# Performance work log

Measured on AMD Instinct MI355X. Metric: run time of the kernel, lower is better.

Reference implementation:

```python
import jax, jax.numpy as jnp
import numpy as np

BN_EPS = 1e-5


def _batchnorm(x, gamma, beta):
    # training-mode BatchNorm2d: biased batch stats over (N, H, W)
    mean = jnp.mean(x, axis=(0, 2, 3), keepdims=True)
    var = jnp.var(x, axis=(0, 2, 3), keepdims=True)
    xn = (x - mean) * jax.lax.rsqrt(var + BN_EPS)
    return xn * gamma[None, :, None, None] + beta[None, :, None, None]


def _bin_weight(w):
    # BitConv2d_Robust: w_bin = sign(w) * mean(|w|) per output channel (STE in fwd is just the value)
    alpha = jnp.mean(jnp.abs(w), axis=(1, 2, 3), keepdims=True)
    return jax.lax.stop_gradient(jnp.sign(w) * alpha - w) + w


def _conv(x, w, b, pad):
    y = jax.lax.conv_general_dilated(
        x, w, window_strides=(1, 1), padding=[(pad, pad), (pad, pad)],
        dimension_numbers=('NCHW', 'OIHW', 'NCHW'))
    return y + b[None, :, None, None]


def setup_inputs() -> dict:
    key = jax.random.key(0)
    ks = jax.random.split(key, 14)
    B, Cin, Cout, T, H, W = 16, 128, 256, 512, 64, 64
    fan1 = Cin * 9
    fan2 = Cout * 9
    return {
        'x': jax.random.normal(ks[0], (B, Cin, H, W), jnp.float32),
        't': jax.random.normal(ks[1], (B, T), jnp.float32),
        'bn1_g': jnp.ones((Cin,), jnp.float32),
        'bn1_b': jnp.zeros((Cin,), jnp.float32),
        'w1': jax.random.normal(ks[2], (Cout, Cin, 3, 3), jnp.float32) / np.sqrt(fan1),
        'b1': jax.random.normal(ks[3], (Cout,), jnp.float32) * 0.01,
        'tW': jax.random.normal(ks[4], (Cout, T), jnp.float32) / np.sqrt(T),
        'tb': jax.random.normal(ks[5], (Cout,), jnp.float32) * 0.01,
        'bn2_g': jnp.ones((Cout,), jnp.float32),
        'bn2_b': jnp.zeros((Cout,), jnp.float32),
        'w2': jax.random.normal(ks[6], (Cout, Cout, 3, 3), jnp.float32) / np.sqrt(fan2),
        'b2': jax.random.normal(ks[7], (Cout,), jnp.float32) * 0.01,
        'ws': jax.random.normal(ks[8], (Cout, Cin, 1, 1), jnp.float32) / np.sqrt(Cin),
        'bs': jax.random.normal(ks[9], (Cout,), jnp.float32) * 0.01,
    }


def reference(x, t, bn1_g, bn1_b, w1, b1, tW, tb, bn2_g, bn2_b, w2, b2, ws, bs):
    h = jnp.sign(_batchnorm(x, bn1_g, bn1_b))                # BN + sign binarize
    h = _conv(h, _bin_weight(w1), b1, pad=1)                  # binarized 3x3 conv
    temb = t @ tW.T + tb                                      # time MLP -> [B, Cout]
    h = h + temb[:, :, None, None]
    h = jnp.sign(_batchnorm(h, bn2_g, bn2_b))
    h = _conv(h, _bin_weight(w2), b2, pad=1)
    skip = _conv(x, _bin_weight(ws), bs, pad=0)               # 1x1 binarized skip (in_ch != out_ch)
    return h + skip
```

## Files before the change

### kernel.cpp

```cpp
#include <hip/hip_runtime.h>
#include <stdint.h>

typedef unsigned int uint;

#define EPS 1e-5f


__global__ __launch_bounds__(256) void k_bn1_part(const float* __restrict__ x, float* __restrict__ part) {
  int c = blockIdx.x, chunk = blockIdx.y;
  float s = 0.f, s2 = 0.f;
  #pragma unroll
  for (int jb = 0; jb < 2; ++jb) {
    int b = chunk * 2 + jb;
    const float4* xb = (const float4*)(x + (((size_t)((b << 7) | c)) << 12));
    #pragma unroll
    for (int k = 0; k < 4; ++k) {
      float4 q = xb[k * 256 + threadIdx.x];
      s += (q.x + q.y) + (q.z + q.w);
      s2 += q.x * q.x + q.y * q.y + q.z * q.z + q.w * q.w;
    }
  }
  #pragma unroll
  for (int off = 32; off > 0; off >>= 1) { s += __shfl_down(s, off); s2 += __shfl_down(s2, off); }
  __shared__ float ls[4], ls2[4];
  int wid = threadIdx.x >> 6, lane = threadIdx.x & 63;
  if (lane == 0) { ls[wid] = s; ls2[wid] = s2; }
  __syncthreads();
  if (threadIdx.x == 0) {
    part[(c * 8 + chunk) * 2 + 0] = ls[0] + ls[1] + ls[2] + ls[3];
    part[(c * 8 + chunk) * 2 + 1] = ls2[0] + ls2[1] + ls2[2] + ls2[3];
  }
}

__global__ void k_bn1_fin(const float* __restrict__ part, const float* __restrict__ g,
                          const float* __restrict__ be, float* __restrict__ sc, float* __restrict__ sh) {
  int c = threadIdx.x;
  float s = 0.f, s2 = 0.f;
  for (int k = 0; k < 8; ++k) { s += part[(c * 8 + k) * 2]; s2 += part[(c * 8 + k) * 2 + 1]; }
  const float inv = 1.f / 65536.f;
  float m = s * inv, var = s2 * inv - m * m;
  float rs = rsqrtf(var + EPS);
  float scale = rs * g[c];
  sc[c] = scale;
  sh[c] = be[c] - m * scale;
}

__global__ __launch_bounds__(128) void k_packw1(const float* __restrict__ w1, uint* __restrict__ wb,
                                                float* __restrict__ alpha) {
  int co = blockIdx.x, wid = threadIdx.x >> 6, lane = threadIdx.x & 63;
  const float* wp = w1 + (co * 128 + threadIdx.x) * 9;
  float wv[9]; float s = 0.f;
  #pragma unroll
  for (int tp = 0; tp < 9; ++tp) { wv[tp] = wp[tp]; s += fabsf(wv[tp]); }
  #pragma unroll
  for (int tp = 0; tp < 9; ++tp) {
    unsigned long long m = __ballot(wv[tp] > 0.f);
    if (lane == 0) {
      wb[(co * 9 + tp) * 4 + wid * 2 + 0] = (uint)m;
      wb[(co * 9 + tp) * 4 + wid * 2 + 1] = (uint)(m >> 32);
    }
  }
  #pragma unroll
  for (int off = 32; off > 0; off >>= 1) s += __shfl_down(s, off);
  __shared__ float l2[2];
  if (lane == 0) l2[wid] = s;
  __syncthreads();
  if (threadIdx.x == 0) alpha[co] = (l2[0] + l2[1]) * (1.f / 1152.f);
}

__global__ __launch_bounds__(256) void k_packw2(const float* __restrict__ w2, uint* __restrict__ wb,
                                                float* __restrict__ alpha) {
  int co = blockIdx.x, wid = threadIdx.x >> 6, lane = threadIdx.x & 63;
  const float* wp = w2 + (co * 256 + threadIdx.x) * 9;
  float wv[9]; float s = 0.f;
  #pragma unroll
  for (int tp = 0; tp < 9; ++tp) { wv[tp] = wp[tp]; s += fabsf(wv[tp]); }
  #pragma unroll
  for (int tp = 0; tp < 9; ++tp) {
    unsigned long long m = __ballot(wv[tp] > 0.f);
    if (lane == 0) {
      wb[(co * 9 + tp) * 8 + wid * 2 + 0] = (uint)m;
      wb[(co * 9 + tp) * 8 + wid * 2 + 1] = (uint)(m >> 32);
    }
  }
  #pragma unroll
  for (int off = 32; off > 0; off >>= 1) s += __shfl_down(s, off);
  __shared__ float l4[4];
  if (lane == 0) l4[wid] = s;
  __syncthreads();
  if (threadIdx.x == 0) alpha[co] = (l4[0] + l4[1] + l4[2] + l4[3]) * (1.f / 2304.f);
}

__global__ __launch_bounds__(256) void k_base(const uint* __restrict__ wb1, const uint* __restrict__ wb2,
                                              int* __restrict__ base1, int* __restrict__ base2) {
  int co = threadIdx.x;
  int pc1[9], pc2[9];
  #pragma unroll
  for (int tp = 0; tp < 9; ++tp) {
    uint a = 0;
    #pragma unroll
    for (int k = 0; k < 4; ++k) a += __popc(wb1[co * 36 + tp * 4 + k]);
    pc1[tp] = (int)a;
    uint b = 0;
    #pragma unroll
    for (int k = 0; k < 8; ++k) b += __popc(wb2[co * 72 + tp * 8 + k]);
    pc2[tp] = (int)b;
  }
  #pragma unroll
  for (int pat = 0; pat < 9; ++pat) {
    int yt = pat / 3, xt = pat % 3;
    int b1v = 1152, b2v = 2304;
    #pragma unroll
    for (int tp = 0; tp < 9; ++tp) {
      int dy = tp / 3 - 1, dx = tp % 3 - 1;
      bool inv = (dy < 0 && yt == 0) || (dy > 0 && yt == 2) || (dx < 0 && xt == 0) || (dx > 0 && xt == 2);
      if (inv) { b1v -= 128 - 2 * pc1[tp]; b2v -= 256 - 2 * pc2[tp]; }
    }
    base1[pat * 256 + co] = b1v;
    base2[pat * 256 + co] = b2v;
  }
}

__global__ __launch_bounds__(128) void k_packws(const float* __restrict__ wsk, float* __restrict__ swT) {
  int co = blockIdx.x, ci = threadIdx.x;
  float v = wsk[co * 128 + ci];
  float s = fabsf(v);
  #pragma unroll
  for (int off = 32; off > 0; off >>= 1) s += __shfl_down(s, off);
  __shared__ float l2[2]; __shared__ float tot;
  int wid = threadIdx.x >> 6, lane = threadIdx.x & 63;
  if (lane == 0) l2[wid] = s;
  __syncthreads();
  if (threadIdx.x == 0) tot = (l2[0] + l2[1]) * (1.f / 128.f);
  __syncthreads();
  float a = tot;
  swT[ci * 256 + co] = (v > 0.f) ? a : -a;
}

__global__ __launch_bounds__(256) void k_temb(const float* __restrict__ t, const float* __restrict__ tW,
                                              const float* __restrict__ tbias, float* __restrict__ temb) {
  int b = blockIdx.x, co = threadIdx.x;
  const float* tr = t + b * 512;
  const float* wr = tW + co * 512;
  float a0 = 0, a1 = 0, a2 = 0, a3 = 0;
  #pragma unroll 8
  for (int k = 0; k < 512; k += 4) {
    a0 = fmaf(tr[k + 0], wr[k + 0], a0);
    a1 = fmaf(tr[k + 1], wr[k + 1], a1);
    a2 = fmaf(tr[k + 2], wr[k + 2], a2);
    a3 = fmaf(tr[k + 3], wr[k + 3], a3);
  }
  temb[b * 256 + co] = (a0 + a1) + (a2 + a3) + tbias[co];
}

__global__ __launch_bounds__(256, 2) void k_skip(const float* __restrict__ x, const float* __restrict__ swT,
                                                 const float* __restrict__ bsk, const float* __restrict__ b2,
                                                 const float* __restrict__ sc1, const float* __restrict__ sh1,
                                                 uint* __restrict__ sbinw, float* __restrict__ out) {
  __shared__ float xs[128 * 64];
  __shared__ float wsl[128 * 64];
  int g = blockIdx.x;
  int b = g >> 6;
  int px0 = (g & 63) << 6;
  int co0 = blockIdx.y << 6;
  int t = threadIdx.x;

  {
    const float* xb = x + ((size_t)(b << 7) << 12) + px0;
    float4* xs4 = (float4*)xs;
    #pragma unroll
    for (int k = 0; k < 8; ++k) {
      int idx = k * 256 + t;
      int ci = idx >> 4, f4 = idx & 15;
      xs4[idx] = *(const float4*)(xb + ((size_t)ci << 12) + (f4 << 2));
    }
  }
  {
    float4* ws4 = (float4*)wsl;
    #pragma unroll
    for (int k = 0; k < 8; ++k) {
      int idx = k * 256 + t;
      int ci = idx >> 4, f4 = idx & 15;
      ws4[idx] = *(const float4*)(swT + ci * 256 + co0 + (f4 << 2));
    }
  }
  __syncthreads();

  if (blockIdx.y == 0) {
    int px = t & 63, wd = t >> 6;
    int ci0 = wd << 5;
    uint acc = 0;
    #pragma unroll
    for (int i = 0; i < 32; ++i) {
      int ci = ci0 + i;
      float v = xs[ci * 64 + px];
      acc |= ((v * sc1[ci] + sh1[ci]) > 0.f ? 1u : 0u) << i;
    }
    sbinw[(((size_t)b << 12) | (px0 + px)) * 4 + wd] = acc;
  }

  int tx = t & 15, ty = t >> 4;
  const float4* xs4 = (const float4*)xs;
  const float4* ws4 = (const float4*)wsl;
  float4 acc0 = make_float4(0, 0, 0, 0), acc1 = acc0, acc2 = acc0, acc3 = acc0;
  #pragma unroll 4
  for (int ci = 0; ci < 128; ++ci) {
    float4 xv = xs4[ci * 16 + tx];
    float4 wv = ws4[ci * 16 + ty];
    acc0.x = fmaf(wv.x, xv.x, acc0.x); acc0.y = fmaf(wv.x, xv.y, acc0.y);
    acc0.z = fmaf(wv.x, xv.z, acc0.z); acc0.w = fmaf(wv.x, xv.w, acc0.w);
    acc1.x = fmaf(wv.y, xv.x, acc1.x); acc1.y = fmaf(wv.y, xv.y, acc1.y);
    acc1.z = fmaf(wv.y, xv.z, acc1.z); acc1.w = fmaf(wv.y, xv.w, acc1.w);
    acc2.x = fmaf(wv.z, xv.x, acc2.x); acc2.y = fmaf(wv.z, xv.y, acc2.y);
    acc2.z = fmaf(wv.z, xv.z, acc2.z); acc2.w = fmaf(wv.z, xv.w, acc2.w);
    acc3.x = fmaf(wv.w, xv.x, acc3.x); acc3.y = fmaf(wv.w, xv.y, acc3.y);
    acc3.z = fmaf(wv.w, xv.z, acc3.z); acc3.w = fmaf(wv.w, xv.w, acc3.w);
  }

  float* op = out + ((size_t)b << 20) + px0 + (tx << 2);
  int cob = co0 + (ty << 2);
  float4 r;
  r = acc0; { float bb = bsk[cob + 0] + b2[cob + 0]; r.x += bb; r.y += bb; r.z += bb; r.w += bb; }
  *(float4*)(op + (size_t)(cob + 0) * 4096) = r;
  r = acc1; { float bb = bsk[cob + 1] + b2[cob + 1]; r.x += bb; r.y += bb; r.z += bb; r.w += bb; }
  *(float4*)(op + (size_t)(cob + 1) * 4096) = r;
  r = acc2; { float bb = bsk[cob + 2] + b2[cob + 2]; r.x += bb; r.y += bb; r.z += bb; r.w += bb; }
  *(float4*)(op + (size_t)(cob + 2) * 4096) = r;
  r = acc3; { float bb = bsk[cob + 3] + b2[cob + 3]; r.x += bb; r.y += bb; r.z += bb; r.w += bb; }
  *(float4*)(op + (size_t)(cob + 3) * 4096) = r;
}

__global__ __launch_bounds__(256, 1) void k_conv1(const uint4* __restrict__ sbin, const uint* __restrict__ wb1,
                                                  const int* __restrict__ base1, short* __restrict__ S1) {
  __shared__ uint wlds[32 * 36];
  __shared__ int blds[9 * 32];
  int co0 = blockIdx.y << 5;
  #pragma unroll
  for (int k = 0; k < 4; ++k) wlds[k * 256 + threadIdx.x] = wb1[co0 * 36 + k * 256 + threadIdx.x];
  if (threadIdx.x < 128) wlds[1024 + threadIdx.x] = wb1[co0 * 36 + 1024 + threadIdx.x];
  #pragma unroll
  for (int k = 0; k < 2; ++k) {
    int idx = k * 256 + threadIdx.x;
    if (idx < 288) blds[idx] = base1[(idx >> 5) * 256 + co0 + (idx & 31)];
  }

  int bt = blockIdx.x;
  int b = bt >> 4;
  int y = ((bt & 15) << 2) | (threadIdx.x >> 6);
  int cx = threadIdx.x & 63;
  uint nb[9][4];
  #pragma unroll
  for (int dy = -1; dy <= 1; ++dy)
    #pragma unroll
    for (int dx = -1; dx <= 1; ++dx) {
      int tp = (dy + 1) * 3 + (dx + 1);
      int yy = y + dy, xx = cx + dx;
      bool v = ((unsigned)yy < 64u) && ((unsigned)xx < 64u);
      uint4 q = make_uint4(0, 0, 0, 0);
      if (v) q = sbin[(b << 12) | (yy << 6) | xx];
      nb[tp][0] = q.x; nb[tp][1] = q.y; nb[tp][2] = q.z; nb[tp][3] = q.w;
    }
  int pat = ((y == 0) ? 0 : ((y == 63) ? 6 : 3)) + ((cx == 0) ? 0 : ((cx == 63) ? 2 : 1));
  __syncthreads();

  int p = (y << 6) | cx;
  short* op = S1 + ((size_t)b << 20) + ((size_t)co0 << 12) + p;
  #pragma unroll 1
  for (int cc = 0; cc < 4; ++cc) {
    short accv[8];
    #pragma unroll
    for (int j = 0; j < 8; ++j) {
      int co_l = cc * 8 + j;
      const uint4* wp4 = (const uint4*)(wlds + co_l * 36);
      uint m0 = 0, m1 = 0, m2 = 0, m3 = 0;
      #pragma unroll
      for (int tp = 0; tp < 9; ++tp) {
        uint4 w4 = wp4[tp];
        m0 += __popc(nb[tp][0] ^ w4.x);
        m1 += __popc(nb[tp][1] ^ w4.y);
        m2 += __popc(nb[tp][2] ^ w4.z);
        m3 += __popc(nb[tp][3] ^ w4.w);
      }
      accv[j] = (short)(blds[pat * 32 + co_l] - 2 * (int)((m0 + m1) + (m2 + m3)));
    }
    #pragma unroll
    for (int j = 0; j < 8; ++j) op[(size_t)(cc * 8 + j) << 12] = accv[j];
  }
}

__global__ __launch_bounds__(256) void k_bn2_part(const short* __restrict__ S1, const float* __restrict__ al1,
                                                  const float* __restrict__ b1, const float* __restrict__ temb,
                                                  float* __restrict__ part) {
  int co = blockIdx.x, chunk = blockIdx.y;
  float a = al1[co], bb = b1[co];
  float s = 0.f, s2 = 0.f;
  #pragma unroll
  for (int jb = 0; jb < 2; ++jb) {
    int b = chunk * 2 + jb;
    float tb_ = bb + temb[(b << 8) | co];
    const uint4* sp = (const uint4*)(S1 + ((size_t)b << 20) + ((size_t)co << 12));
    #pragma unroll
    for (int k = 0; k < 2; ++k) {
      uint4 q = sp[k * 256 + threadIdx.x];
      uint ws[4] = {q.x, q.y, q.z, q.w};
      #pragma unroll
      for (int w = 0; w < 4; ++w) {
        float f0 = fmaf(a, (float)((short)(ws[w] & 0xffffu)), tb_);
        float f1 = fmaf(a, (float)((short)(ws[w] >> 16)), tb_);
        s += f0 + f1;
        s2 += f0 * f0 + f1 * f1;
      }
    }
  }
  #pragma unroll
  for (int off = 32; off > 0; off >>= 1) { s += __shfl_down(s, off); s2 += __shfl_down(s2, off); }
  __shared__ float ls[4], ls2[4];
  int wid = threadIdx.x >> 6, lane = threadIdx.x & 63;
  if (lane == 0) { ls[wid] = s; ls2[wid] = s2; }
  __syncthreads();
  if (threadIdx.x == 0) {
    part[(co * 8 + chunk) * 2 + 0] = ls[0] + ls[1] + ls[2] + ls[3];
    part[(co * 8 + chunk) * 2 + 1] = ls2[0] + ls2[1] + ls2[2] + ls2[3];
  }
}

__global__ void k_bn2_fin(const float* __restrict__ part, const float* __restrict__ al1,
                          const float* __restrict__ b1, const float* __restrict__ g2,
                          const float* __restrict__ be2, float* __restrict__ A,
                          float* __restrict__ Bc, float* __restrict__ Cc) {
  int co = threadIdx.x;
  float s = 0.f, s2 = 0.f;
  for (int k = 0; k < 8; ++k) { s += part[(co * 8 + k) * 2]; s2 += part[(co * 8 + k) * 2 + 1]; }
  const float inv = 1.f / 65536.f;
  float m = s * inv, var = s2 * inv - m * m;
  float rs = rsqrtf(var + EPS);
  float gg = rs * g2[co];
  A[co] = al1[co] * gg;
  Bc[co] = (b1[co] - m) * gg + be2[co];
  Cc[co] = gg;
}

__global__ __launch_bounds__(256) void k_bin2(const short* __restrict__ S1, const float* __restrict__ A,
                                              const float* __restrict__ Bc, const float* __restrict__ Cc,
                                              const float* __restrict__ temb, uint4* __restrict__ hbin) {
  int pg = blockIdx.x * 256 + threadIdx.x;
  int b = pg >> 12, p = pg & 4095;
  int c0 = blockIdx.y << 7;
  const short* sp = S1 + ((size_t)b << 20) + p;
  const float* tp = temb + (b << 8);
  uint w[4];
  #pragma unroll
  for (int wd = 0; wd < 4; ++wd) {
    uint acc = 0;
    #pragma unroll
    for (int i = 0; i < 32; ++i) {
      int co = c0 + wd * 32 + i;
      float v = A[co] * (float)sp[(size_t)co << 12] + Bc[co] + Cc[co] * tp[co];
      acc |= (v > 0.f ? 1u : 0u) << i;
    }
    w[wd] = acc;
  }
  hbin[pg * 2 + blockIdx.y] = make_uint4(w[0], w[1], w[2], w[3]);
}

__global__ __launch_bounds__(256, 1) void k_conv2(const uint4* __restrict__ hbin, const uint* __restrict__ wb2,
                                                  const int* __restrict__ base2, const float* __restrict__ al2,
                                                  float* __restrict__ out) {
  __shared__ uint wlds[32 * 72];
  __shared__ int blds[9 * 32];
  int co0 = blockIdx.y << 5;
  #pragma unroll
  for (int k = 0; k < 9; ++k) wlds[k * 256 + threadIdx.x] = wb2[co0 * 72 + k * 256 + threadIdx.x];
  #pragma unroll
  for (int k = 0; k < 2; ++k) {
    int idx = k * 256 + threadIdx.x;
    if (idx < 288) blds[idx] = base2[(idx >> 5) * 256 + co0 + (idx & 31)];
  }

  int bt = blockIdx.x;
  int b = bt >> 4;
  int y = ((bt & 15) << 2) | (threadIdx.x >> 6);
  int cx = threadIdx.x & 63;
  uint nb[9][8];
  #pragma unroll
  for (int dy = -1; dy <= 1; ++dy)
    #pragma unroll
    for (int dx = -1; dx <= 1; ++dx) {
      int tp = (dy + 1) * 3 + (dx + 1);
      int yy = y + dy, xx = cx + dx;
      bool v = ((unsigned)yy < 64u) && ((unsigned)xx < 64u);
      uint4 q0 = make_uint4(0, 0, 0, 0), q1 = make_uint4(0, 0, 0, 0);
      if (v) {
        int pix = (b << 12) | (yy << 6) | xx;
        q0 = hbin[pix * 2 + 0];
        q1 = hbin[pix * 2 + 1];
      }
      nb[tp][0] = q0.x; nb[tp][1] = q0.y; nb[tp][2] = q0.z; nb[tp][3] = q0.w;
      nb[tp][4] = q1.x; nb[tp][5] = q1.y; nb[tp][6] = q1.z; nb[tp][7] = q1.w;
    }
  int pat = ((y == 0) ? 0 : ((y == 63) ? 6 : 3)) + ((cx == 0) ? 0 : ((cx == 63) ? 2 : 1));
  __syncthreads();

  int p = (y << 6) | cx;
  float* op = out + ((size_t)b << 20) + ((size_t)co0 << 12) + p;
  #pragma unroll 1
  for (int cc = 0; cc < 4; ++cc) {
    float ov[8];
    #pragma unroll
    for (int j = 0; j < 8; ++j) ov[j] = op[(size_t)(cc * 8 + j) << 12];
    #pragma unroll
    for (int j = 0; j < 8; ++j) {
      int co_l = cc * 8 + j;
      const uint4* wp4 = (const uint4*)(wlds + co_l * 72);
      uint m0 = 0, m1 = 0, m2 = 0, m3 = 0;
      #pragma unroll
      for (int tp = 0; tp < 9; ++tp) {
        uint4 wa = wp4[tp * 2 + 0];
        uint4 wb_ = wp4[tp * 2 + 1];
        m0 += __popc(nb[tp][0] ^ wa.x);
        m1 += __popc(nb[tp][1] ^ wa.y);
        m2 += __popc(nb[tp][2] ^ wa.z);
        m3 += __popc(nb[tp][3] ^ wa.w);
        m0 += __popc(nb[tp][4] ^ wb_.x);
        m1 += __popc(nb[tp][5] ^ wb_.y);
        m2 += __popc(nb[tp][6] ^ wb_.z);
        m3 += __popc(nb[tp][7] ^ wb_.w);
      }
      int acc = blds[pat * 32 + co_l] - 2 * (int)((m0 + m1) + (m2 + m3));
      ov[j] = fmaf(al2[co0 + co_l], (float)acc, ov[j]);
    }
    #pragma unroll
    for (int j = 0; j < 8; ++j) op[(size_t)(cc * 8 + j) << 12] = ov[j];
  }
}

extern "C" void kernel_launch(void* const* d_in, const int* in_sizes, int n_in,
                              void* d_out, int out_size, void* d_ws, size_t ws_size,
                              hipStream_t stream) {
  const float* x    = (const float*)d_in[0];
  const float* t    = (const float*)d_in[1];
  const float* bn1g = (const float*)d_in[2];
  const float* bn1b = (const float*)d_in[3];
  const float* w1   = (const float*)d_in[4];
  const float* b1   = (const float*)d_in[5];
  const float* tW   = (const float*)d_in[6];
  const float* tb   = (const float*)d_in[7];
  const float* bn2g = (const float*)d_in[8];
  const float* bn2b = (const float*)d_in[9];
  const float* w2   = (const float*)d_in[10];
  const float* b2   = (const float*)d_in[11];
  const float* wsk  = (const float*)d_in[12];
  const float* bsk  = (const float*)d_in[13];
  float* out = (float*)d_out;
  char* ws = (char*)d_ws;

  float* bn1part = (float*)(ws + 0);
  float* sc1     = (float*)(ws + 8192);
  float* sh1     = (float*)(ws + 8704);
  uint4* sbin    = (uint4*)(ws + 9216);
  uint*  wb1     = (uint*) (ws + 1057792);
  float* al1     = (float*)(ws + 1094656);
  uint*  wb2     = (uint*) (ws + 1095680);
  float* al2     = (float*)(ws + 1169408);
  float* swkT    = (float*)(ws + 1170432);
  float* temb    = (float*)(ws + 1301504);
  float* bn2part = (float*)(ws + 1317888);
  float* A2      = (float*)(ws + 1334272);
  float* Bc2     = (float*)(ws + 1335296);
  float* Cc2     = (float*)(ws + 1336320);
  uint4* hbin    = (uint4*)(ws + 1337344);
  int*   base1g  = (int*)  (ws + 3434496);
  int*   base2g  = (int*)  (ws + 3443712);
  short* S1      = (short*)(ws + 3452928);

  k_bn1_part<<<dim3(128, 8), 256, 0, stream>>>(x, bn1part);
  k_bn1_fin<<<1, 128, 0, stream>>>(bn1part, bn1g, bn1b, sc1, sh1);
  k_packw1<<<256, 128, 0, stream>>>(w1, wb1, al1);
  k_packw2<<<256, 256, 0, stream>>>(w2, wb2, al2);
  k_base<<<1, 256, 0, stream>>>(wb1, wb2, base1g, base2g);
  k_packws<<<256, 128, 0, stream>>>(wsk, swkT);
  k_temb<<<16, 256, 0, stream>>>(t, tW, tb, temb);
  k_skip<<<dim3(1024, 4), 256, 0, stream>>>(x, swkT, bsk, b2, sc1, sh1, (uint*)sbin, out);
  k_conv1<<<dim3(256, 8), 256, 0, stream>>>(sbin, wb1, base1g, S1);
  k_bn2_part<<<dim3(256, 8), 256, 0, stream>>>(S1, al1, b1, temb, bn2part);
  k_bn2_fin<<<1, 256, 0, stream>>>(bn2part, al1, b1, bn2g, bn2b, A2, Bc2, Cc2);
  k_bin2<<<dim3(256, 2), 256, 0, stream>>>(S1, A2, Bc2, Cc2, temb, hbin);
  k_conv2<<<dim3(256, 8), 256, 0, stream>>>(hbin, wb2, base2g, al2, out);
}
```

Before: 259.7 us.

## Read binary conv weights via uniform global loads and raise occupancy in conv kernels

```diff
diff --git a/kernel.cpp b/kernel.cpp
--- a/kernel.cpp
+++ b/kernel.cpp
@@ -230,19 +230,12 @@
   *(float4*)(op + (size_t)(cob + 3) * 4096) = r;
 }
 
-__global__ __launch_bounds__(256, 1) void k_conv1(const uint4* __restrict__ sbin, const uint* __restrict__ wb1,
+__global__ __launch_bounds__(256, 4) void k_conv1(const uint4* __restrict__ sbin, const uint* __restrict__ wb1,
                                                   const int* __restrict__ base1, short* __restrict__ S1) {
-  __shared__ uint wlds[32 * 36];
   __shared__ int blds[9 * 32];
   int co0 = blockIdx.y << 5;
-  #pragma unroll
-  for (int k = 0; k < 4; ++k) wlds[k * 256 + threadIdx.x] = wb1[co0 * 36 + k * 256 + threadIdx.x];
-  if (threadIdx.x < 128) wlds[1024 + threadIdx.x] = wb1[co0 * 36 + 1024 + threadIdx.x];
-  #pragma unroll
-  for (int k = 0; k < 2; ++k) {
-    int idx = k * 256 + threadIdx.x;
-    if (idx < 288) blds[idx] = base1[(idx >> 5) * 256 + co0 + (idx & 31)];
-  }
+  if (threadIdx.x < 256) blds[threadIdx.x] = base1[(threadIdx.x >> 5) * 256 + co0 + (threadIdx.x & 31)];
+  if (threadIdx.x < 32) blds[256 + threadIdx.x] = base1[8 * 256 + co0 + threadIdx.x];
 
   int bt = blockIdx.x;
   int b = bt >> 4;
@@ -263,28 +256,31 @@
   int pat = ((y == 0) ? 0 : ((y == 63) ? 6 : 3)) + ((cx == 0) ? 0 : ((cx == 63) ? 2 : 1));
   __syncthreads();
 
+  int accv[32];
+  #pragma unroll
+  for (int co_l = 0; co_l < 32; ++co_l) {
+    const uint4* wp = (const uint4*)(wb1 + (size_t)(co0 + co_l) * 36);
+    uint m0 = 0, m1 = 0, m2 = 0, m3 = 0;
+    #pragma unroll
+    for (int tp = 0; tp < 9; ++tp) {
+      uint4 w4 = wp[tp];
+      m0 += __popc(nb[tp][0] ^ w4.x);
+      m1 += __popc(nb[tp][1] ^ w4.y);
+      m2 += __popc(nb[tp][2] ^ w4.z);
+      m3 += __popc(nb[tp][3] ^ w4.w);
+    }
+    accv[co_l] = (int)((m0 + m1) + (m2 + m3));
+  }
+
   int p = (y << 6) | cx;
   short* op = S1 + ((size_t)b << 20) + ((size_t)co0 << 12) + p;
   #pragma unroll 1
   for (int cc = 0; cc < 4; ++cc) {
-    short accv[8];
     #pragma unroll
     for (int j = 0; j < 8; ++j) {
       int co_l = cc * 8 + j;
-      const uint4* wp4 = (const uint4*)(wlds + co_l * 36);
-      uint m0 = 0, m1 = 0, m2 = 0, m3 = 0;
-      #pragma unroll
-      for (int tp = 0; tp < 9; ++tp) {
-        uint4 w4 = wp4[tp];
-        m0 += __popc(nb[tp][0] ^ w4.x);
-        m1 += __popc(nb[tp][1] ^ w4.y);
-        m2 += __popc(nb[tp][2] ^ w4.z);
-        m3 += __popc(nb[tp][3] ^ w4.w);
-      }
-      accv[j] = (short)(blds[pat * 32 + co_l] - 2 * (int)((m0 + m1) + (m2 + m3)));
-    }
-    #pragma unroll
-    for (int j = 0; j < 8; ++j) op[(size_t)(cc * 8 + j) << 12] = accv[j];
+      op[(size_t)co_l << 12] = (short)(blds[pat * 32 + co_l] - 2 * accv[co_l]);
+    }
   }
 }
 
@@ -363,43 +359,54 @@
   hbin[pg * 2 + blockIdx.y] = make_uint4(w[0], w[1], w[2], w[3]);
 }
 
-__global__ __launch_bounds__(256, 1) void k_conv2(const uint4* __restrict__ hbin, const uint* __restrict__ wb2,
+__global__ __launch_bounds__(256, 4) void k_conv2(const uint4* __restrict__ hbin, const uint* __restrict__ wb2,
                                                   const int* __restrict__ base2, const float* __restrict__ al2,
                                                   float* __restrict__ out) {
-  __shared__ uint wlds[32 * 72];
   __shared__ int blds[9 * 32];
+  __shared__ float alds[32];
   int co0 = blockIdx.y << 5;
-  #pragma unroll
-  for (int k = 0; k < 9; ++k) wlds[k * 256 + threadIdx.x] = wb2[co0 * 72 + k * 256 + threadIdx.x];
-  #pragma unroll
-  for (int k = 0; k < 2; ++k) {
-    int idx = k * 256 + threadIdx.x;
-    if (idx < 288) blds[idx] = base2[(idx >> 5) * 256 + co0 + (idx & 31)];
-  }
+  if (threadIdx.x < 256) blds[threadIdx.x] = base2[(threadIdx.x >> 5) * 256 + co0 + (threadIdx.x & 31)];
+  if (threadIdx.x < 32) blds[256 + threadIdx.x] = base2[8 * 256 + co0 + threadIdx.x];
+  if (threadIdx.x >= 32 && threadIdx.x < 64) alds[threadIdx.x - 32] = al2[co0 + threadIdx.x - 32];
 
   int bt = blockIdx.x;
   int b = bt >> 4;
   int y = ((bt & 15) << 2) | (threadIdx.x >> 6);
   int cx = threadIdx.x & 63;
-  uint nb[9][8];
-  #pragma unroll
-  for (int dy = -1; dy <= 1; ++dy)
-    #pragma unroll
-    for (int dx = -1; dx <= 1; ++dx) {
-      int tp = (dy + 1) * 3 + (dx + 1);
-      int yy = y + dy, xx = cx + dx;
-      bool v = ((unsigned)yy < 64u) && ((unsigned)xx < 64u);
-      uint4 q0 = make_uint4(0, 0, 0, 0), q1 = make_uint4(0, 0, 0, 0);
-      if (v) {
-        int pix = (b << 12) | (yy << 6) | xx;
-        q0 = hbin[pix * 2 + 0];
-        q1 = hbin[pix * 2 + 1];
+  int pat = ((y == 0) ? 0 : ((y == 63) ? 6 : 3)) + ((cx == 0) ? 0 : ((cx == 63) ? 2 : 1));
+  __syncthreads();
+
+  int accv[32];
+  #pragma unroll
+  for (int hc = 0; hc < 2; ++hc) {
+    uint nb[9][4];
+    #pragma unroll
+    for (int dy = -1; dy <= 1; ++dy)
+      #pragma unroll
+      for (int dx = -1; dx <= 1; ++dx) {
+        int tp = (dy + 1) * 3 + (dx + 1);
+        int yy = y + dy, xx = cx + dx;
+        bool v = ((unsigned)yy < 64u) && ((unsigned)xx < 64u);
+        uint4 q = make_uint4(0, 0, 0, 0);
+        if (v) q = hbin[(((b << 12) | (yy << 6) | xx) << 1) + hc];
+        nb[tp][0] = q.x; nb[tp][1] = q.y; nb[tp][2] = q.z; nb[tp][3] = q.w;
       }
-      nb[tp][0] = q0.x; nb[tp][1] = q0.y; nb[tp][2] = q0.z; nb[tp][3] = q0.w;
-      nb[tp][4] = q1.x; nb[tp][5] = q1.y; nb[tp][6] = q1.z; nb[tp][7] = q1.w;
-    }
-  int pat = ((y == 0) ? 0 : ((y == 63) ? 6 : 3)) + ((cx == 0) ? 0 : ((cx == 63) ? 2 : 1));
-  __syncthreads();
+    #pragma unroll
+    for (int co_l = 0; co_l < 32; ++co_l) {
+      const uint4* wp = (const uint4*)(wb2 + (size_t)(co0 + co_l) * 72) + hc;
+      uint m0 = 0, m1 = 0, m2 = 0, m3 = 0;
+      #pragma unroll
+      for (int tp = 0; tp < 9; ++tp) {
+        uint4 w4 = wp[tp * 2];
+        m0 += __popc(nb[tp][0] ^ w4.x);
+        m1 += __popc(nb[tp][1] ^ w4.y);
+        m2 += __popc(nb[tp][2] ^ w4.z);
+        m3 += __popc(nb[tp][3] ^ w4.w);
+      }
+      int mm = (int)((m0 + m1) + (m2 + m3));
+      if (hc == 0) accv[co_l] = mm; else accv[co_l] += mm;
+    }
+  }
 
   int p = (y << 6) | cx;
   float* op = out + ((size_t)b << 20) + ((size_t)co0 << 12) + p;
@@ -411,23 +418,8 @@
     #pragma unroll
     for (int j = 0; j < 8; ++j) {
       int co_l = cc * 8 + j;
-      const uint4* wp4 = (const uint4*)(wlds + co_l * 72);
-      uint m0 = 0, m1 = 0, m2 = 0, m3 = 0;
-      #pragma unroll
-      for (int tp = 0; tp < 9; ++tp) {
-        uint4 wa = wp4[tp * 2 + 0];
-        uint4 wb_ = wp4[tp * 2 + 1];
-        m0 += __popc(nb[tp][0] ^ wa.x);
-        m1 += __popc(nb[tp][1] ^ wa.y);
-        m2 += __popc(nb[tp][2] ^ wa.z);
-        m3 += __popc(nb[tp][3] ^ wa.w);
-        m0 += __popc(nb[tp][4] ^ wb_.x);
-        m1 += __popc(nb[tp][5] ^ wb_.y);
-        m2 += __popc(nb[tp][6] ^ wb_.z);
-        m3 += __popc(nb[tp][7] ^ wb_.w);
-      }
-      int acc = blds[pat * 32 + co_l] - 2 * (int)((m0 + m1) + (m2 + m3));
-      ov[j] = fmaf(al2[co0 + co_l], (float)acc, ov[j]);
+      int acc = blds[pat * 32 + co_l] - 2 * accv[co_l];
+      ov[j] = fmaf(alds[co_l], (float)acc, ov[j]);
     }
     #pragma unroll
     for (int j = 0; j < 8; ++j) op[(size_t)(cc * 8 + j) << 12] = ov[j];
```

Measured after the change: 518.2 us. +99.5%, slower.

## Replace popcount conv2 with bf16 MFMA conv on ±1 activations and weights

Applied to the files above, without the earlier changes.

```diff
diff --git a/kernel.cpp b/kernel.cpp
--- a/kernel.cpp
+++ b/kernel.cpp
@@ -2,6 +2,8 @@
 #include <stdint.h>
 
 typedef unsigned int uint;
+typedef short bf16x8 __attribute__((ext_vector_type(8)));
+typedef float f32x4 __attribute__((ext_vector_type(4)));
 
 #define EPS 1e-5f
 
@@ -69,7 +71,7 @@
 }
 
 __global__ __launch_bounds__(256) void k_packw2(const float* __restrict__ w2, uint* __restrict__ wb,
-                                                float* __restrict__ alpha) {
+                                                float* __restrict__ alpha, ushort* __restrict__ wsgn2) {
   int co = blockIdx.x, wid = threadIdx.x >> 6, lane = threadIdx.x & 63;
   const float* wp = w2 + (co * 256 + threadIdx.x) * 9;
   float wv[9]; float s = 0.f;
@@ -77,6 +79,7 @@
   for (int tp = 0; tp < 9; ++tp) { wv[tp] = wp[tp]; s += fabsf(wv[tp]); }
   #pragma unroll
   for (int tp = 0; tp < 9; ++tp) {
+    wsgn2[(co * 9 + tp) * 256 + threadIdx.x] = (wv[tp] > 0.f) ? 0x3F80u : 0xBF80u;
     unsigned long long m = __ballot(wv[tp] > 0.f);
     if (lane == 0) {
       wb[(co * 9 + tp) * 8 + wid * 2 + 0] = (uint)m;
@@ -340,9 +343,120 @@
   Cc[co] = gg;
 }
 
-__global__ __launch_bounds__(256) void k_bin2(const short* __restrict__ S1, const float* __restrict__ A,
-                                              const float* __restrict__ Bc, const float* __restrict__ Cc,
-                                              const float* __restrict__ temb, uint4* __restrict__ hbin) {
+__global__ __launch_bounds__(256) void k_bin2_bf16(const short* __restrict__ S1, const float* __restrict__ A,
+                                                   const float* __restrict__ Bc, const float* __restrict__ Cc,
+                                                   const float* __restrict__ temb, uint4* __restrict__ h2u4) {
+  __shared__ uint4 tile[64 * 32];
+  int b = blockIdx.x >> 6;
+  int px0 = (blockIdx.x & 63) << 6;
+  int pxl = threadIdx.x & 63, quad = threadIdx.x >> 6;
+  const short* sp = S1 + ((size_t)b << 20) + (px0 + pxl);
+  const float* tp = temb + (b << 8);
+  #pragma unroll 1
+  for (int g = 0; g < 8; ++g) {
+    uint d[4];
+    #pragma unroll
+    for (int h = 0; h < 4; ++h) {
+      int c0 = quad * 64 + g * 8 + h * 2;
+      float v0 = A[c0] * (float)sp[(size_t)c0 << 12] + Bc[c0] + Cc[c0] * tp[c0];
+      float v1 = A[c0 + 1] * (float)sp[(size_t)(c0 + 1) << 12] + Bc[c0 + 1] + Cc[c0 + 1] * tp[c0 + 1];
+      uint s0 = (v0 > 0.f) ? 0x3F80u : 0xBF80u;
+      uint s1 = (v1 > 0.f) ? 0x3F80u : 0xBF80u;
+      d[h] = s0 | (s1 << 16);
+    }
+    int slot = quad * 8 + g;
+    tile[pxl * 32 + (slot ^ (pxl & 7))] = make_uint4(d[0], d[1], d[2], d[3]);
+  }
+  __syncthreads();
+  uint4* dst = h2u4 + ((size_t)(b << 12) + px0) * 32;
+  #pragma unroll
+  for (int k = 0; k < 8; ++k) {
+    int c = k * 256 + threadIdx.x;
+    int px = c >> 5, slot = c & 31;
+    dst[c] = tile[px * 32 + (slot ^ (px & 7))];
+  }
+}
+
+__global__ __launch_bounds__(256, 2) void k_conv2_mfma(const ushort* __restrict__ h2,
+                                                       const ushort* __restrict__ wsgn2,
+                                                       const float* __restrict__ al2,
+                                                       float* __restrict__ out) {
+  __shared__ ushort act[3 * 66 * 136];
+  int bidx = blockIdx.x;
+  int s = (bidx & 7) * 128 + (bidx >> 3);
+  int b = s >> 6, y = s & 63;
+  int lane = threadIdx.x & 63, wave = threadIdx.x >> 6;
+  int co0 = wave << 6;
+  int l15 = lane & 15, lk = lane >> 4;
+
+  f32x4 acc[4][4] = {};
+
+  const uint4* h2g = (const uint4*)h2;
+  uint4* a4 = (uint4*)act;
+
+  #pragma unroll 1
+  for (int chunk = 0; chunk < 2; ++chunk) {
+    if (chunk) __syncthreads();
+    #pragma unroll 1
+    for (int i = 0; i < 13; ++i) {
+      int idx = i * 256 + threadIdx.x;
+      if (idx < 3168) {
+        int q = idx & 15, xz = (idx >> 4) % 66, r = (idx >> 4) / 66;
+        int yy = y + r - 1, xx = xz - 1;
+        uint4 v = make_uint4(0, 0, 0, 0);
+        if (((unsigned)yy < 64u) && ((unsigned)xx < 64u))
+          v = h2g[(size_t)(((b << 12) | (yy << 6) | xx)) * 32 + chunk * 16 + q];
+        a4[(r * 66 + xz) * 17 + q] = v;
+      }
+    }
+    __syncthreads();
+
+    #pragma unroll 1
+    for (int tp = 0; tp < 9; ++tp) {
+      int rbase = (tp / 3) * 66 + (tp % 3);
+      size_t wbase = (size_t)(tp * 256 + chunk * 128 + lk * 8);
+      #pragma unroll
+      for (int kc = 0; kc < 4; ++kc) {
+        bf16x8 Bv[4];
+        #pragma unroll
+        for (int pt = 0; pt < 4; ++pt) {
+          int xi = rbase + pt * 16 + l15;
+          Bv[pt] = *(bf16x8*)&act[xi * 136 + kc * 32 + lk * 8];
+        }
+        bf16x8 Av[4];
+        #pragma unroll
+        for (int ct = 0; ct < 4; ++ct) {
+          int co = co0 + ct * 16 + l15;
+          Av[ct] = *(const bf16x8*)(wsgn2 + (size_t)co * 2304 + wbase + kc * 32);
+        }
+        #pragma unroll
+        for (int ct = 0; ct < 4; ++ct)
+          #pragma unroll
+          for (int pt = 0; pt < 4; ++pt)
+            acc[ct][pt] = __builtin_amdgcn_mfma_f32_16x16x32_bf16(Av[ct], Bv[pt], acc[ct][pt], 0, 0, 0);
+      }
+    }
+  }
+
+  float* ob = out + ((size_t)b << 20) + (y << 6);
+  #pragma unroll
+  for (int ct = 0; ct < 4; ++ct) {
+    #pragma unroll
+    for (int pt = 0; pt < 4; ++pt) {
+      int x = pt * 16 + l15;
+      #pragma unroll
+      for (int r = 0; r < 4; ++r) {
+        int co = co0 + ct * 16 + lk * 4 + r;
+        float* p = ob + ((size_t)co << 12) + x;
+        *p = fmaf(al2[co], acc[ct][pt][r], *p);
+      }
+    }
+  }
+}
+
+__global__ __launch_bounds__(256) void k_bin2_packed(const short* __restrict__ S1, const float* __restrict__ A,
+                                                     const float* __restrict__ Bc, const float* __restrict__ Cc,
+                                                     const float* __restrict__ temb, uint4* __restrict__ hbin) {
   int pg = blockIdx.x * 256 + threadIdx.x;
   int b = pg >> 12, p = pg & 4095;
   int c0 = blockIdx.y << 7;
@@ -363,9 +477,9 @@
   hbin[pg * 2 + blockIdx.y] = make_uint4(w[0], w[1], w[2], w[3]);
 }
 
-__global__ __launch_bounds__(256, 1) void k_conv2(const uint4* __restrict__ hbin, const uint* __restrict__ wb2,
-                                                  const int* __restrict__ base2, const float* __restrict__ al2,
-                                                  float* __restrict__ out) {
+__global__ __launch_bounds__(256, 1) void k_conv2_pop(const uint4* __restrict__ hbin, const uint* __restrict__ wb2,
+                                                      const int* __restrict__ base2, const float* __restrict__ al2,
+                                                      float* __restrict__ out) {
   __shared__ uint wlds[32 * 72];
   __shared__ int blds[9 * 32];
   int co0 = blockIdx.y << 5;
@@ -376,7 +490,6 @@
     int idx = k * 256 + threadIdx.x;
     if (idx < 288) blds[idx] = base2[(idx >> 5) * 256 + co0 + (idx & 31)];
   }
-
   int bt = blockIdx.x;
   int b = bt >> 4;
   int y = ((bt & 15) << 2) | (threadIdx.x >> 6);
@@ -468,15 +581,19 @@
   float* A2      = (float*)(ws + 1334272);
   float* Bc2     = (float*)(ws + 1335296);
   float* Cc2     = (float*)(ws + 1336320);
-  uint4* hbin    = (uint4*)(ws + 1337344);
-  int*   base1g  = (int*)  (ws + 3434496);
-  int*   base2g  = (int*)  (ws + 3443712);
-  short* S1      = (short*)(ws + 3452928);
+  int*   base1g  = (int*)  (ws + 1337344);
+  int*   base2g  = (int*)  (ws + 1346560);
+  uint4* hbin    = (uint4*)(ws + 1355776);
+  ushort* wsgn2  = (ushort*)(ws + 3452928);
+  short* S1      = (short*)(ws + 4632576);
+  ushort* h2     = (ushort*)(ws + 38187008);
+  const size_t WS_NEED_MFMA = 71741440ULL;
+  bool use_mfma = (ws_size >= WS_NEED_MFMA);
 
   k_bn1_part<<<dim3(128, 8), 256, 0, stream>>>(x, bn1part);
   k_bn1_fin<<<1, 128, 0, stream>>>(bn1part, bn1g, bn1b, sc1, sh1);
   k_packw1<<<256, 128, 0, stream>>>(w1, wb1, al1);
-  k_packw2<<<256, 256, 0, stream>>>(w2, wb2, al2);
+  k_packw2<<<256, 256, 0, stream>>>(w2, wb2, al2, wsgn2);
   k_base<<<1, 256, 0, stream>>>(wb1, wb2, base1g, base2g);
   k_packws<<<256, 128, 0, stream>>>(wsk, swkT);
   k_temb<<<16, 256, 0, stream>>>(t, tW, tb, temb);
@@ -484,6 +601,11 @@
   k_conv1<<<dim3(256, 8), 256, 0, stream>>>(sbin, wb1, base1g, S1);
   k_bn2_part<<<dim3(256, 8), 256, 0, stream>>>(S1, al1, b1, temb, bn2part);
   k_bn2_fin<<<1, 256, 0, stream>>>(bn2part, al1, b1, bn2g, bn2b, A2, Bc2, Cc2);
-  k_bin2<<<dim3(256, 2), 256, 0, stream>>>(S1, A2, Bc2, Cc2, temb, hbin);
-  k_conv2<<<dim3(256, 8), 256, 0, stream>>>(hbin, wb2, base2g, al2, out);
-}
+  if (use_mfma) {
+    k_bin2_bf16<<<1024, 256, 0, stream>>>(S1, A2, Bc2, Cc2, temb, (uint4*)h2);
+    k_conv2_mfma<<<1024, 256, 0, stream>>>(h2, wsgn2, al2, out);
+  } else {
+    k_bin2_packed<<<dim3(256, 2), 256, 0, stream>>>(S1, A2, Bc2, Cc2, temb, hbin);
+    k_conv2_pop<<<dim3(256, 8), 256, 0, stream>>>(hbin, wb2, base2g, al2, out);
+  }
+}
```

Result: slower. 323.1 us (+24.4%).
